# Kernel optimization log

Measured on AMD Instinct MI355X. Metric: run time of the kernel, lower is better.

## Reference

```python
import jax, jax.numpy as jnp
import numpy as np

N, E, L = 50000, 800000, 200000
IN_FEATS, HID = 256, 128
EPS = 1e-5


def setup_inputs() -> dict:
    key = jax.random.key(0)
    ks = jax.random.split(key, 32)
    def lin(k, fan_in, fan_out):
        s = 1.0 / np.sqrt(fan_in)
        return jax.random.uniform(k, (fan_out, fan_in), jnp.float32, -s, s)
    inp = {
        "x": jax.random.normal(ks[0], (N, IN_FEATS), jnp.float32),
        "edge_index": jax.random.randint(ks[1], (2, E), 0, N, jnp.int32),
        "edge_label_index": jax.random.randint(ks[2], (2, L), 0, N, jnp.int32),
        # SAGEConv layers: lin_l (on aggregated neighbors, with bias), lin_r (root, no bias)
        "w1l": lin(ks[3], IN_FEATS, HID), "b1l": jnp.zeros((HID,), jnp.float32), "w1r": lin(ks[4], IN_FEATS, HID),
        "w2l": lin(ks[5], HID, HID), "b2l": jnp.zeros((HID,), jnp.float32), "w2r": lin(ks[6], HID, HID),
        "w3l": lin(ks[7], HID, HID), "b3l": jnp.zeros((HID,), jnp.float32), "w3r": lin(ks[8], HID, HID),
        # BatchNorm (eval mode: running stats)
        "bn1_g": jnp.ones((HID,), jnp.float32), "bn1_b": jnp.zeros((HID,), jnp.float32),
        "bn1_m": 0.1 * jax.random.normal(ks[9], (HID,), jnp.float32),
        "bn1_v": jax.random.uniform(ks[10], (HID,), jnp.float32, 0.5, 1.5),
        "bn2_g": jnp.ones((HID,), jnp.float32), "bn2_b": jnp.zeros((HID,), jnp.float32),
        "bn2_m": 0.1 * jax.random.normal(ks[11], (HID,), jnp.float32),
        "bn2_v": jax.random.uniform(ks[12], (HID,), jnp.float32, 0.5, 1.5),
        # Decoder MLP
        "dw1": lin(ks[13], 2 * HID, HID), "db1": jnp.zeros((HID,), jnp.float32),
        "dw2": lin(ks[14], HID, 1), "db2": jnp.zeros((1,), jnp.float32),
    }
    return inp


def _sage_conv(x, src, dst, wl, bl, wr):
    # mean-aggregate neighbor features at dst, then lin_l(agg) + lin_r(x)
    n = x.shape[0]
    agg = jax.ops.segment_sum(x[src], dst, num_segments=n)
    cnt = jax.ops.segment_sum(jnp.ones_like(dst, dtype=x.dtype), dst, num_segments=n)
    mean = agg / jnp.maximum(cnt, 1.0)[:, None]
    return mean @ wl.T + bl + x @ wr.T


def _bn_eval(h, g, b, m, v):
    return (h - m) * (g * jax.lax.rsqrt(v + EPS)) + b


def reference(x, edge_index, edge_label_index,
              w1l, b1l, w1r, w2l, b2l, w2r, w3l, b3l, w3r,
              bn1_g, bn1_b, bn1_m, bn1_v, bn2_g, bn2_b, bn2_m, bn2_v,
              dw1, db1, dw2, db2):
    src, dst = edge_index[0], edge_index[1]
    h = _sage_conv(x, src, dst, w1l, b1l, w1r)
    h = jax.nn.relu(_bn_eval(h, bn1_g, bn1_b, bn1_m, bn1_v))
    h = _sage_conv(h, src, dst, w2l, b2l, w2r)
    h = jax.nn.relu(_bn_eval(h, bn2_g, bn2_b, bn2_m, bn2_v))
    z = _sage_conv(h, src, dst, w3l, b3l, w3r)
    # decode: gather pair embeddings, concat, MLP -> scalar per pair
    s, d = edge_label_index[0], edge_label_index[1]
    pair = jnp.concatenate([z[s], z[d]], axis=1)  # [L, 2*HID]
    hdec = jax.nn.relu(pair @ dw1.T + db1)
    return (hdec @ dw2.T + db2).reshape(-1)
```

## Files before the change

### kernel.cpp

```cpp
#include <hip/hip_runtime.h>
#include <hip/hip_fp16.h>


typedef unsigned int uint;
using s16x8 = __attribute__((ext_vector_type(8))) short;
using f32x4 = __attribute__((ext_vector_type(4))) float;

__device__ inline void bsplit(float v, ushort& hi, ushort& lo) {
    uint u = __float_as_uint(v);
    uint hb = (u + 0x7FFFu + ((u >> 16) & 1u)) >> 16;
    hi = (ushort)hb;
    float r = v - __uint_as_float(hb << 16);
    uint u2 = __float_as_uint(r);
    lo = (ushort)((u2 + 0x7FFFu + ((u2 >> 16) & 1u)) >> 16);
}

__device__ inline ushort f2h(float v) { return __half_as_ushort(__float2half(v)); }

__device__ inline float4 h4f(uint2 r) {
    float2 fa = __half22float2(*(const __half2*)&r.x);
    float2 fb = __half22float2(*(const __half2*)&r.y);
    return make_float4(fa.x, fa.y, fb.x, fb.y);
}

__device__ inline uint swz(uint i, uint r) {
    return (i & ~63u) | ((i ^ (r << 3)) & 56u) | (i & 7u);
}

__device__ inline void gload16(const void* g, void* l) {
    __builtin_amdgcn_global_load_lds(
        (const __attribute__((address_space(1))) unsigned int*)g,
        (__attribute__((address_space(3))) unsigned int*)l, 16, 0, 0);
}

__global__ void count_kernel(const int* __restrict__ dst, int* __restrict__ cnt,
                             int* __restrict__ rank, int E) {
    int i = blockIdx.x * blockDim.x + threadIdx.x;
    if (i < E) rank[i] = atomicAdd(&cnt[dst[i]], 1);
}

__global__ void scanA_kernel(const int* __restrict__ cnt, int* __restrict__ ptr,
                             int* __restrict__ tilesum, int n) {
    __shared__ int sd[1024];
    int t = threadIdx.x;
    int i = blockIdx.x * 1024 + t;
    int v = (i < n) ? cnt[i] : 0;
    sd[t] = v;
    __syncthreads();
    #pragma unroll
    for (int off = 1; off < 1024; off <<= 1) {
        int add = (t >= off) ? sd[t - off] : 0;
        __syncthreads();
        sd[t] += add;
        __syncthreads();
    }
    if (i < n) ptr[i] = sd[t] - v;
    if (t == 1023) tilesum[blockIdx.x] = sd[t];
}

__global__ void scanB_kernel(int* __restrict__ tilesum, int* __restrict__ ptr,
                             int ntiles, int n) {
    if (threadIdx.x == 0 && blockIdx.x == 0) {
        int running = 0;
        for (int b = 0; b < ntiles; ++b) {
            int t = tilesum[b];
            tilesum[b] = running;
            running += t;
        }
        ptr[n] = running;
    }
}

__global__ void scanC_kernel(int* __restrict__ ptr, const int* __restrict__ tilesum, int n) {
    int i = blockIdx.x * blockDim.x + threadIdx.x;
    if (i < n) ptr[i] += tilesum[i >> 10];
}

__global__ void scatter_kernel(const int* __restrict__ src, const int* __restrict__ dst,
                               const int* __restrict__ ptr, const int* __restrict__ rank,
                               int* __restrict__ edges, int E) {
    int i = blockIdx.x * blockDim.x + threadIdx.x;
    if (i < E) edges[ptr[dst[i]] + rank[i]] = src[i];
}

__global__ __launch_bounds__(256) void convx_kernel(const float* __restrict__ x,
                                                    ushort* __restrict__ A3, int total) {
    int e = blockIdx.x * 256 + threadIdx.x;
    if (e >= total) return;
    uint row = e >> 6;
    uint k4 = (e & 63) << 2;
    float4 v = *(const float4*)(x + (size_t)row * 256 + k4);
    ushort4 hi, lo;
    bsplit(v.x, hi.x, lo.x); bsplit(v.y, hi.y, lo.y);
    bsplit(v.z, hi.z, lo.z); bsplit(v.w, hi.w, lo.w);
    ushort* d = A3 + (size_t)row * 512;
    *(ushort4*)(d + swz(k4, row))       = hi;
    *(ushort4*)(d + swz(k4 + 256, row)) = lo;
}

__global__ void wprep_all_kernel(
    const float* __restrict__ w1l, const float* __restrict__ w1r,
    const float* __restrict__ w2l, const float* __restrict__ w2r,
    const float* __restrict__ w3l, const float* __restrict__ w3r,
    const float* __restrict__ dw1,
    ushort* __restrict__ WS1, ushort* __restrict__ WS2,
    ushort* __restrict__ WS3, ushort* __restrict__ WS4)
{
    int which = blockIdx.y;
    uint n = blockIdx.x;
    uint k = threadIdx.x;
    const float *wa, *wb;
    uint K, lda, aoff, boff;
    ushort* WS;
    switch (which) {
        case 0:  wa = w1l; wb = w1r; K = 256; lda = 256; aoff = 0; boff = 0;   WS = WS1; break;
        case 1:  wa = w2l; wb = w2r; K = 128; lda = 128; aoff = 0; boff = 0;   WS = WS2; break;
        case 2:  wa = w3l; wb = w3r; K = 128; lda = 128; aoff = 0; boff = 0;   WS = WS3; break;
        default: wa = dw1; wb = dw1; K = 128; lda = 256; aoff = 0; boff = 128; WS = WS4; break;
    }
    if (k >= K) return;
    const float* srcr = (n < 128) ? (wa + (size_t)n * lda + aoff)
                                  : (wb + (size_t)(n - 128) * lda + boff);
    ushort hi, lo;
    bsplit(srcr[k], hi, lo);
    ushort* d = WS + (size_t)n * 3 * K;
    d[swz(k, n)]         = hi;
    d[swz(K + k, n)]     = lo;
    d[swz(2 * K + k, n)] = hi;
}

template <int KP, int CRF16>
__global__ __launch_bounds__(256, 2) void mm_kernel(const ushort* __restrict__ A,
                                                    const ushort* __restrict__ WS,
                                                    ushort* __restrict__ Cl,
                                                    void* __restrict__ Cr_, int M) {
    constexpr int KS  = (KP / 64) + (KP / 128);
    constexpr int WKP = KP + KP / 2;
    __shared__ ushort At[128 * 64];
    __shared__ ushort Bt[256 * 64];
    const int t = threadIdx.x;
    const int lane = t & 63;
    const int wave = t >> 6;
    const int wm = wave >> 1, wn = wave & 1;
    const int row0 = blockIdx.x * 128;
    const int l15 = lane & 15;
    const int l4 = lane >> 4;
    const int l8 = lane >> 3;
    const int c8 = lane & 7;

    f32x4 acc[4][8] = {};

    for (int s = 0; s < KS; ++s) {
        const int as = (s < KP / 128) ? s : s - (KP / 128);
        #pragma unroll
        for (int j = 0; j < 4; ++j) {
            int jj = wave + j * 4;
            int r = jj * 8 + l8;
            gload16(A + (size_t)(row0 + r) * KP + as * 64 + c8 * 8,
                    (char*)At + jj * 1024 + lane * 16);
        }
        #pragma unroll
        for (int j = 0; j < 8; ++j) {
            int jj = wave + j * 4;
            int r = jj * 8 + l8;
            gload16(WS + (size_t)r * WKP + s * 64 + c8 * 8,
                    (char*)Bt + jj * 1024 + lane * 16);
        }
        __syncthreads();
        #pragma unroll
        for (int kk = 0; kk < 64; kk += 32) {
            s16x8 af[4], bf[8];
            #pragma unroll
            for (int mi = 0; mi < 4; ++mi) {
                int r = wm * 64 + mi * 16 + l15;
                int off = (kk + l4 * 8) ^ ((r & 7) * 8);
                af[mi] = *(const s16x8*)&At[r * 64 + off];
            }
            #pragma unroll
            for (int ni = 0; ni < 8; ++ni) {
                int r = wn * 128 + ni * 16 + l15;
                int off = (kk + l4 * 8) ^ ((r & 7) * 8);
                bf[ni] = *(const s16x8*)&Bt[r * 64 + off];
            }
            #pragma unroll
            for (int mi = 0; mi < 4; ++mi)
                #pragma unroll
                for (int ni = 0; ni < 8; ++ni)
                    acc[mi][ni] = __builtin_amdgcn_mfma_f32_16x16x32_bf16(
                        af[mi], bf[ni], acc[mi][ni], 0, 0, 0);
        }
        __syncthreads();
    }
    #pragma unroll
    for (int mi = 0; mi < 4; ++mi) {
        int rbase = row0 + wm * 64 + mi * 16 + l4 * 4;
        #pragma unroll
        for (int ni = 0; ni < 8; ++ni) {
            int col = ni * 16 + l15;
            #pragma unroll
            for (int j = 0; j < 4; ++j) {
                int r = rbase + j;
                if (r < M) {
                    if (wn == 0) {
                        Cl[(size_t)r * 128 + col] = f2h(acc[mi][ni][j]);
                    } else if (CRF16) {
                        ((ushort*)Cr_)[(size_t)r * 128 + col] = f2h(acc[mi][ni][j]);
                    } else {
                        ((float*)Cr_)[(size_t)r * 128 + col] = acc[mi][ni][j];
                    }
                }
            }
        }
    }
}

__global__ __launch_bounds__(256, 4) void agg_kernel(
    const ushort* __restrict__ tl, const float* __restrict__ tr,
    const int* __restrict__ ptr, const int* __restrict__ edges,
    const float* __restrict__ bl,
    const float* __restrict__ bng, const float* __restrict__ bnb,
    const float* __restrict__ bnm, const float* __restrict__ bnv,
    int do_bn, ushort* __restrict__ h3, int n) {
    const int wave = threadIdx.x >> 6;
    const int lane = threadIdx.x & 63;
    const uint node = blockIdx.x * 4 + wave;
    if (node >= (uint)n) return;
    const int half = lane >> 5;
    const uint q4 = (lane & 31) << 2;
    const int p0 = ptr[node], p1 = ptr[node + 1];
    float4 a0 = make_float4(0.f, 0.f, 0.f, 0.f), a1 = a0, a2 = a0, a3 = a0;
    float4 a4 = a0, a5 = a0, a6 = a0, a7 = a0;
    int e = p0 + half;
    for (; e + 14 < p1; e += 16) {
        int i0 = edges[e],      i1 = edges[e + 2],  i2 = edges[e + 4],  i3 = edges[e + 6];
        int i4 = edges[e + 8],  i5 = edges[e + 10], i6 = edges[e + 12], i7 = edges[e + 14];
        uint2 r0 = *(const uint2*)(tl + (size_t)i0 * 128 + q4);
        uint2 r1 = *(const uint2*)(tl + (size_t)i1 * 128 + q4);
        uint2 r2 = *(const uint2*)(tl + (size_t)i2 * 128 + q4);
        uint2 r3 = *(const uint2*)(tl + (size_t)i3 * 128 + q4);
        uint2 r4 = *(const uint2*)(tl + (size_t)i4 * 128 + q4);
        uint2 r5 = *(const uint2*)(tl + (size_t)i5 * 128 + q4);
        uint2 r6 = *(const uint2*)(tl + (size_t)i6 * 128 + q4);
        uint2 r7 = *(const uint2*)(tl + (size_t)i7 * 128 + q4);
        float4 v0 = h4f(r0), v1 = h4f(r1), v2 = h4f(r2), v3 = h4f(r3);
        float4 v4 = h4f(r4), v5 = h4f(r5), v6 = h4f(r6), v7 = h4f(r7);
        a0.x += v0.x; a0.y += v0.y; a0.z += v0.z; a0.w += v0.w;
        a1.x += v1.x; a1.y += v1.y; a1.z += v1.z; a1.w += v1.w;
        a2.x += v2.x; a2.y += v2.y; a2.z += v2.z; a2.w += v2.w;
        a3.x += v3.x; a3.y += v3.y; a3.z += v3.z; a3.w += v3.w;
        a4.x += v4.x; a4.y += v4.y; a4.z += v4.z; a4.w += v4.w;
        a5.x += v5.x; a5.y += v5.y; a5.z += v5.z; a5.w += v5.w;
        a6.x += v6.x; a6.y += v6.y; a6.z += v6.z; a6.w += v6.w;
        a7.x += v7.x; a7.y += v7.y; a7.z += v7.z; a7.w += v7.w;
    }
    for (; e < p1; e += 2) {
        int i0 = edges[e];
        float4 v0 = h4f(*(const uint2*)(tl + (size_t)i0 * 128 + q4));
        a0.x += v0.x; a0.y += v0.y; a0.z += v0.z; a0.w += v0.w;
    }
    float4 s;
    s.x = ((a0.x + a1.x) + (a2.x + a3.x)) + ((a4.x + a5.x) + (a6.x + a7.x));
    s.y = ((a0.y + a1.y) + (a2.y + a3.y)) + ((a4.y + a5.y) + (a6.y + a7.y));
    s.z = ((a0.z + a1.z) + (a2.z + a3.z)) + ((a4.z + a5.z) + (a6.z + a7.z));
    s.w = ((a0.w + a1.w) + (a2.w + a3.w)) + ((a4.w + a5.w) + (a6.w + a7.w));
    s.x += __shfl_xor(s.x, 32);
    s.y += __shfl_xor(s.y, 32);
    s.z += __shfl_xor(s.z, 32);
    s.w += __shfl_xor(s.w, 32);
    if (half == 0) {
        float inv = 1.f / fmaxf((float)(p1 - p0), 1.f);
        float4 r = *(const float4*)(tr + (size_t)node * 128 + q4);
        float4 b = *(const float4*)(bl + q4);
        float4 val;
        val.x = fmaf(s.x, inv, b.x) + r.x;
        val.y = fmaf(s.y, inv, b.y) + r.y;
        val.z = fmaf(s.z, inv, b.z) + r.z;
        val.w = fmaf(s.w, inv, b.w) + r.w;
        if (do_bn) {
            float4 g = *(const float4*)(bng + q4);
            float4 be = *(const float4*)(bnb + q4);
            float4 m = *(const float4*)(bnm + q4);
            float4 vv = *(const float4*)(bnv + q4);
            val.x = fmaxf(fmaf(val.x - m.x, g.x * rsqrtf(vv.x + 1e-5f), be.x), 0.f);
            val.y = fmaxf(fmaf(val.y - m.y, g.y * rsqrtf(vv.y + 1e-5f), be.y), 0.f);
            val.z = fmaxf(fmaf(val.z - m.z, g.z * rsqrtf(vv.z + 1e-5f), be.z), 0.f);
            val.w = fmaxf(fmaf(val.w - m.w, g.w * rsqrtf(vv.w + 1e-5f), be.w), 0.f);
        }
        ushort4 hi, lo;
        bsplit(val.x, hi.x, lo.x); bsplit(val.y, hi.y, lo.y);
        bsplit(val.z, hi.z, lo.z); bsplit(val.w, hi.w, lo.w);
        ushort* d = h3 + (size_t)node * 256;
        *(ushort4*)(d + swz(q4, node))       = hi;
        *(ushort4*)(d + swz(q4 + 128, node)) = lo;
    }
}

__global__ __launch_bounds__(256) void decode_kernel(
    const ushort* __restrict__ u, const ushort* __restrict__ v,
    const int* __restrict__ eli, const float* __restrict__ db1,
    const float* __restrict__ dw2, const float* __restrict__ db2,
    float* __restrict__ out, int L) {
    __shared__ float sb[128], sw[128];
    if (threadIdx.x < 128) {
        sb[threadIdx.x] = db1[threadIdx.x];
        sw[threadIdx.x] = dw2[threadIdx.x];
    }
    __syncthreads();
    int p = blockIdx.x * 256 + threadIdx.x;
    if (p >= L) return;
    int s = eli[p], d = eli[L + p];
    const ushort* up = u + (size_t)s * 128;
    const ushort* vp = v + (size_t)d * 128;
    float acc = db2[0];
    #pragma unroll 8
    for (int o = 0; o < 128; o += 4) {
        float4 a = h4f(*(const uint2*)(up + o));
        float4 b = h4f(*(const uint2*)(vp + o));
        float4 bb = *(const float4*)(&sb[o]);
        float4 w = *(const float4*)(&sw[o]);
        acc += fmaxf(a.x + b.x + bb.x, 0.f) * w.x;
        acc += fmaxf(a.y + b.y + bb.y, 0.f) * w.y;
        acc += fmaxf(a.z + b.z + bb.z, 0.f) * w.z;
        acc += fmaxf(a.w + b.w + bb.w, 0.f) * w.w;
    }
    out[p] = acc;
}

extern "C" void kernel_launch(void* const* d_in, const int* in_sizes, int n_in,
                              void* d_out, int out_size, void* d_ws, size_t ws_size,
                              hipStream_t stream) {
    const float* x    = (const float*)d_in[0];
    const int*   ei   = (const int*)d_in[1];
    const int*   eli  = (const int*)d_in[2];
    const float* w1l  = (const float*)d_in[3];
    const float* b1l  = (const float*)d_in[4];
    const float* w1r  = (const float*)d_in[5];
    const float* w2l  = (const float*)d_in[6];
    const float* b2l  = (const float*)d_in[7];
    const float* w2r  = (const float*)d_in[8];
    const float* w3l  = (const float*)d_in[9];
    const float* b3l  = (const float*)d_in[10];
    const float* w3r  = (const float*)d_in[11];
    const float* bn1g = (const float*)d_in[12];
    const float* bn1b = (const float*)d_in[13];
    const float* bn1m = (const float*)d_in[14];
    const float* bn1v = (const float*)d_in[15];
    const float* bn2g = (const float*)d_in[16];
    const float* bn2b = (const float*)d_in[17];
    const float* bn2m = (const float*)d_in[18];
    const float* bn2v = (const float*)d_in[19];
    const float* dw1  = (const float*)d_in[20];
    const float* db1  = (const float*)d_in[21];
    const float* dw2  = (const float*)d_in[22];
    const float* db2  = (const float*)d_in[23];
    float* out = (float*)d_out;

    const int N = in_sizes[0] / 256;
    const int E = in_sizes[1] / 2;
    const int L = in_sizes[2] / 2;
    const int* src = ei;
    const int* dst = ei + E;
    const int ntiles = (N + 1023) >> 10;
    const int nblk = (N + 127) / 128;
    const int Npad = nblk * 128;

    char* wsb = (char*)d_ws;
    size_t off = 0;
    auto carve = [&](size_t bytes) -> void* {
        void* p = wsb + off;
        off += (bytes + 255) & ~(size_t)255;
        return p;
    };
    int* ptr        = (int*)carve((size_t)(N + 1) * 4);
    int* cnt        = (int*)carve((size_t)N * 4);
    int* rank       = (int*)carve((size_t)E * 4);
    int* tilesum    = (int*)carve((size_t)ntiles * 4);
    int* edges      = (int*)carve((size_t)E * 4);
    ushort* WS1     = (ushort*)carve((size_t)256 * 768 * 2);
    ushort* WS2     = (ushort*)carve((size_t)256 * 384 * 2);
    ushort* WS3     = (ushort*)carve((size_t)256 * 384 * 2);
    ushort* WS4     = (ushort*)carve((size_t)256 * 384 * 2);
    ushort* tl_h    = (ushort*)carve((size_t)N * 128 * 2);
    float* tr_c     = (float*)carve((size_t)N * 128 * 4);
    ushort* A3      = (ushort*)carve((size_t)Npad * 512 * 2);
    ushort* h3      = A3;

    hipMemsetAsync(cnt, 0, (size_t)N * 4, stream);
    count_kernel<<<(E + 255) / 256, 256, 0, stream>>>(dst, cnt, rank, E);
    scanA_kernel<<<ntiles, 1024, 0, stream>>>(cnt, ptr, tilesum, N);
    scanB_kernel<<<1, 64, 0, stream>>>(tilesum, ptr, ntiles, N);
    scanC_kernel<<<(N + 255) / 256, 256, 0, stream>>>(ptr, tilesum, N);
    scatter_kernel<<<(E + 255) / 256, 256, 0, stream>>>(src, dst, ptr, rank, edges, E);

    convx_kernel<<<(N * 64 + 255) / 256, 256, 0, stream>>>(x, A3, N * 64);
    wprep_all_kernel<<<dim3(256, 4), 256, 0, stream>>>(w1l, w1r, w2l, w2r, w3l, w3r,
                                                       dw1, WS1, WS2, WS3, WS4);

    mm_kernel<512, 0><<<nblk, 256, 0, stream>>>(A3, WS1, tl_h, tr_c, N);
    agg_kernel<<<(N + 3) / 4, 256, 0, stream>>>(tl_h, tr_c, ptr, edges, b1l,
                                                bn1g, bn1b, bn1m, bn1v, 1, h3, N);
    mm_kernel<256, 0><<<nblk, 256, 0, stream>>>(h3, WS2, tl_h, tr_c, N);
    agg_kernel<<<(N + 3) / 4, 256, 0, stream>>>(tl_h, tr_c, ptr, edges, b2l,
                                                bn2g, bn2b, bn2m, bn2v, 1, h3, N);
    mm_kernel<256, 0><<<nblk, 256, 0, stream>>>(h3, WS3, tl_h, tr_c, N);
    agg_kernel<<<(N + 3) / 4, 256, 0, stream>>>(tl_h, tr_c, ptr, edges, b3l,
                                                bn1g, bn1b, bn1m, bn1v, 0, h3, N);
    mm_kernel<256, 1><<<nblk, 256, 0, stream>>>(h3, WS4, tl_h, tr_c, N);
    decode_kernel<<<(L + 255) / 256, 256, 0, stream>>>(tl_h, (const ushort*)tr_c, eli,
                                                       db1, dw2, db2, out, L);
}
```

Before: 366.5 us.

## Merge prep kernels into one launch and prefetch edge indices in aggregation

New measurement: 360.0 us. About the same (-1.8%).

```diff
diff --git a/kernel.cpp b/kernel.cpp
--- a/kernel.cpp
+++ b/kernel.cpp
@@ -33,10 +33,57 @@
         (__attribute__((address_space(3))) unsigned int*)l, 16, 0, 0);
 }
 
-__global__ void count_kernel(const int* __restrict__ dst, int* __restrict__ cnt,
-                             int* __restrict__ rank, int E) {
-    int i = blockIdx.x * blockDim.x + threadIdx.x;
-    if (i < E) rank[i] = atomicAdd(&cnt[dst[i]], 1);
+__global__ __launch_bounds__(256) void prep_kernel(
+    const float* __restrict__ x, ushort* __restrict__ A3, int totalconv, int nconv,
+    const int* __restrict__ dst, int* __restrict__ cnt, int* __restrict__ rank,
+    int E, int ncount,
+    const float* __restrict__ w1l, const float* __restrict__ w1r,
+    const float* __restrict__ w2l, const float* __restrict__ w2r,
+    const float* __restrict__ w3l, const float* __restrict__ w3r,
+    const float* __restrict__ dw1,
+    ushort* __restrict__ WS1, ushort* __restrict__ WS2,
+    ushort* __restrict__ WS3, ushort* __restrict__ WS4)
+{
+    const int bid = blockIdx.x;
+    if (bid < nconv) {
+        int e = bid * 256 + threadIdx.x;
+        if (e >= totalconv) return;
+        uint row = e >> 6;
+        uint k4 = (e & 63) << 2;
+        float4 v = *(const float4*)(x + (size_t)row * 256 + k4);
+        ushort4 hi, lo;
+        bsplit(v.x, hi.x, lo.x); bsplit(v.y, hi.y, lo.y);
+        bsplit(v.z, hi.z, lo.z); bsplit(v.w, hi.w, lo.w);
+        ushort* d = A3 + (size_t)row * 512;
+        *(ushort4*)(d + swz(k4, row))       = hi;
+        *(ushort4*)(d + swz(k4 + 256, row)) = lo;
+    } else if (bid < nconv + ncount) {
+        int i = (bid - nconv) * 256 + threadIdx.x;
+        if (i < E) rank[i] = atomicAdd(&cnt[dst[i]], 1);
+    } else {
+        int w = bid - nconv - ncount;
+        uint n = w & 255;
+        int which = w >> 8;
+        uint k = threadIdx.x;
+        const float *wa, *wb;
+        uint K, lda, aoff, boff;
+        ushort* WS;
+        switch (which) {
+            case 0:  wa = w1l; wb = w1r; K = 256; lda = 256; aoff = 0; boff = 0;   WS = WS1; break;
+            case 1:  wa = w2l; wb = w2r; K = 128; lda = 128; aoff = 0; boff = 0;   WS = WS2; break;
+            case 2:  wa = w3l; wb = w3r; K = 128; lda = 128; aoff = 0; boff = 0;   WS = WS3; break;
+            default: wa = dw1; wb = dw1; K = 128; lda = 256; aoff = 0; boff = 128; WS = WS4; break;
+        }
+        if (k >= K) return;
+        const float* srcr = (n < 128) ? (wa + (size_t)n * lda + aoff)
+                                      : (wb + (size_t)(n - 128) * lda + boff);
+        ushort hi, lo;
+        bsplit(srcr[k], hi, lo);
+        ushort* d = WS + (size_t)n * 3 * K;
+        d[swz(k, n)]         = hi;
+        d[swz(K + k, n)]     = lo;
+        d[swz(2 * K + k, n)] = hi;
+    }
 }
 
 __global__ void scanA_kernel(const int* __restrict__ cnt, int* __restrict__ ptr,
@@ -81,52 +128,6 @@
                                int* __restrict__ edges, int E) {
     int i = blockIdx.x * blockDim.x + threadIdx.x;
     if (i < E) edges[ptr[dst[i]] + rank[i]] = src[i];
-}
-
-__global__ __launch_bounds__(256) void convx_kernel(const float* __restrict__ x,
-                                                    ushort* __restrict__ A3, int total) {
-    int e = blockIdx.x * 256 + threadIdx.x;
-    if (e >= total) return;
-    uint row = e >> 6;
-    uint k4 = (e & 63) << 2;
-    float4 v = *(const float4*)(x + (size_t)row * 256 + k4);
-    ushort4 hi, lo;
-    bsplit(v.x, hi.x, lo.x); bsplit(v.y, hi.y, lo.y);
-    bsplit(v.z, hi.z, lo.z); bsplit(v.w, hi.w, lo.w);
-    ushort* d = A3 + (size_t)row * 512;
-    *(ushort4*)(d + swz(k4, row))       = hi;
-    *(ushort4*)(d + swz(k4 + 256, row)) = lo;
-}
-
-__global__ void wprep_all_kernel(
-    const float* __restrict__ w1l, const float* __restrict__ w1r,
-    const float* __restrict__ w2l, const float* __restrict__ w2r,
-    const float* __restrict__ w3l, const float* __restrict__ w3r,
-    const float* __restrict__ dw1,
-    ushort* __restrict__ WS1, ushort* __restrict__ WS2,
-    ushort* __restrict__ WS3, ushort* __restrict__ WS4)
-{
-    int which = blockIdx.y;
-    uint n = blockIdx.x;
-    uint k = threadIdx.x;
-    const float *wa, *wb;
-    uint K, lda, aoff, boff;
-    ushort* WS;
-    switch (which) {
-        case 0:  wa = w1l; wb = w1r; K = 256; lda = 256; aoff = 0; boff = 0;   WS = WS1; break;
-        case 1:  wa = w2l; wb = w2r; K = 128; lda = 128; aoff = 0; boff = 0;   WS = WS2; break;
-        case 2:  wa = w3l; wb = w3r; K = 128; lda = 128; aoff = 0; boff = 0;   WS = WS3; break;
-        default: wa = dw1; wb = dw1; K = 128; lda = 256; aoff = 0; boff = 128; WS = WS4; break;
-    }
-    if (k >= K) return;
-    const float* srcr = (n < 128) ? (wa + (size_t)n * lda + aoff)
-                                  : (wb + (size_t)(n - 128) * lda + boff);
-    ushort hi, lo;
-    bsplit(srcr[k], hi, lo);
-    ushort* d = WS + (size_t)n * 3 * K;
-    d[swz(k, n)]         = hi;
-    d[swz(K + k, n)]     = lo;
-    d[swz(2 * K + k, n)] = hi;
 }
 
 template <int KP, int CRF16>
@@ -231,17 +232,28 @@
     float4 a0 = make_float4(0.f, 0.f, 0.f, 0.f), a1 = a0, a2 = a0, a3 = a0;
     float4 a4 = a0, a5 = a0, a6 = a0, a7 = a0;
     int e = p0 + half;
-    for (; e + 14 < p1; e += 16) {
-        int i0 = edges[e],      i1 = edges[e + 2],  i2 = edges[e + 4],  i3 = edges[e + 6];
-        int i4 = edges[e + 8],  i5 = edges[e + 10], i6 = edges[e + 12], i7 = edges[e + 14];
-        uint2 r0 = *(const uint2*)(tl + (size_t)i0 * 128 + q4);
-        uint2 r1 = *(const uint2*)(tl + (size_t)i1 * 128 + q4);
-        uint2 r2 = *(const uint2*)(tl + (size_t)i2 * 128 + q4);
-        uint2 r3 = *(const uint2*)(tl + (size_t)i3 * 128 + q4);
-        uint2 r4 = *(const uint2*)(tl + (size_t)i4 * 128 + q4);
-        uint2 r5 = *(const uint2*)(tl + (size_t)i5 * 128 + q4);
-        uint2 r6 = *(const uint2*)(tl + (size_t)i6 * 128 + q4);
-        uint2 r7 = *(const uint2*)(tl + (size_t)i7 * 128 + q4);
+    int i0 = 0, i1 = 0, i2 = 0, i3 = 0, i4 = 0, i5 = 0, i6 = 0, i7 = 0;
+    bool have = (e + 14 < p1);
+    if (have) {
+        i0 = edges[e];      i1 = edges[e + 2];  i2 = edges[e + 4];  i3 = edges[e + 6];
+        i4 = edges[e + 8];  i5 = edges[e + 10]; i6 = edges[e + 12]; i7 = edges[e + 14];
+    }
+    while (have) {
+        int c0 = i0, c1 = i1, c2 = i2, c3 = i3, c4 = i4, c5 = i5, c6 = i6, c7 = i7;
+        e += 16;
+        have = (e + 14 < p1);
+        if (have) {
+            i0 = edges[e];      i1 = edges[e + 2];  i2 = edges[e + 4];  i3 = edges[e + 6];
+            i4 = edges[e + 8];  i5 = edges[e + 10]; i6 = edges[e + 12]; i7 = edges[e + 14];
+        }
+        uint2 r0 = *(const uint2*)(tl + (size_t)c0 * 128 + q4);
+        uint2 r1 = *(const uint2*)(tl + (size_t)c1 * 128 + q4);
+        uint2 r2 = *(const uint2*)(tl + (size_t)c2 * 128 + q4);
+        uint2 r3 = *(const uint2*)(tl + (size_t)c3 * 128 + q4);
+        uint2 r4 = *(const uint2*)(tl + (size_t)c4 * 128 + q4);
+        uint2 r5 = *(const uint2*)(tl + (size_t)c5 * 128 + q4);
+        uint2 r6 = *(const uint2*)(tl + (size_t)c6 * 128 + q4);
+        uint2 r7 = *(const uint2*)(tl + (size_t)c7 * 128 + q4);
         float4 v0 = h4f(r0), v1 = h4f(r1), v2 = h4f(r2), v3 = h4f(r3);
         float4 v4 = h4f(r4), v5 = h4f(r5), v6 = h4f(r6), v7 = h4f(r7);
         a0.x += v0.x; a0.y += v0.y; a0.z += v0.z; a0.w += v0.w;
@@ -253,10 +265,17 @@
         a6.x += v6.x; a6.y += v6.y; a6.z += v6.z; a6.w += v6.w;
         a7.x += v7.x; a7.y += v7.y; a7.z += v7.z; a7.w += v7.w;
     }
-    for (; e < p1; e += 2) {
-        int i0 = edges[e];
-        float4 v0 = h4f(*(const uint2*)(tl + (size_t)i0 * 128 + q4));
+    for (; e + 2 < p1; e += 4) {
+        int c0 = edges[e], c1 = edges[e + 2];
+        float4 v0 = h4f(*(const uint2*)(tl + (size_t)c0 * 128 + q4));
+        float4 v1 = h4f(*(const uint2*)(tl + (size_t)c1 * 128 + q4));
         a0.x += v0.x; a0.y += v0.y; a0.z += v0.z; a0.w += v0.w;
+        a1.x += v1.x; a1.y += v1.y; a1.z += v1.z; a1.w += v1.w;
+    }
+    if (e < p1) {
+        int c0 = edges[e];
+        float4 v0 = h4f(*(const uint2*)(tl + (size_t)c0 * 128 + q4));
+        a2.x += v0.x; a2.y += v0.y; a2.z += v0.z; a2.w += v0.w;
     }
     float4 s;
     s.x = ((a0.x + a1.x) + (a2.x + a3.x)) + ((a4.x + a5.x) + (a6.x + a7.x));
@@ -363,6 +382,8 @@
     const int ntiles = (N + 1023) >> 10;
     const int nblk = (N + 127) / 128;
     const int Npad = nblk * 128;
+    const int nconv = (N * 64 + 255) / 256;
+    const int ncount = (E + 255) / 256;
 
     char* wsb = (char*)d_ws;
     size_t off = 0;
@@ -386,15 +407,13 @@
     ushort* h3      = A3;
 
     hipMemsetAsync(cnt, 0, (size_t)N * 4, stream);
-    count_kernel<<<(E + 255) / 256, 256, 0, stream>>>(dst, cnt, rank, E);
+    prep_kernel<<<nconv + ncount + 1024, 256, 0, stream>>>(
+        x, A3, N * 64, nconv, dst, cnt, rank, E, ncount,
+        w1l, w1r, w2l, w2r, w3l, w3r, dw1, WS1, WS2, WS3, WS4);
     scanA_kernel<<<ntiles, 1024, 0, stream>>>(cnt, ptr, tilesum, N);
     scanB_kernel<<<1, 64, 0, stream>>>(tilesum, ptr, ntiles, N);
     scanC_kernel<<<(N + 255) / 256, 256, 0, stream>>>(ptr, tilesum, N);
     scatter_kernel<<<(E + 255) / 256, 256, 0, stream>>>(src, dst, ptr, rank, edges, E);
-
-    convx_kernel<<<(N * 64 + 255) / 256, 256, 0, stream>>>(x, A3, N * 64);
-    wprep_all_kernel<<<dim3(256, 4), 256, 0, stream>>>(w1l, w1r, w2l, w2r, w3l, w3r,
-                                                       dw1, WS1, WS2, WS3, WS4);
 
     mm_kernel<512, 0><<<nblk, 256, 0, stream>>>(A3, WS1, tl_h, tr_c, N);
     agg_kernel<<<(N + 3) / 4, 256, 0, stream>>>(tl_h, tr_c, ptr, edges, b1l,
```
